# Kernel tuning notes

Hardware: AMD Instinct MI355X
Metric: run time of the kernel (lower is better)

## Reference

```python
import jax, jax.numpy as jnp
import numpy as np

B, N, S, H, W, DG = 16, 64, 4, 32, 32, 8  # batch, base width, scales, spatial, deform groups (=num_cls)
K = 9  # 3x3 kernel
EPS = 1e-5


def conv2d(x, w, b):
    # x: (B,Cin,H,W), w: (Cout,Cin,3,3), stride 1, pad 1
    y = jax.lax.conv_general_dilated(x, w, (1, 1), ((1, 1), (1, 1)),
                                     dimension_numbers=('NCHW', 'OIHW', 'NCHW'))
    return y + b[None, :, None, None]


def bn(x, g, be):
    # BatchNorm2d in training mode: batch stats over (N,H,W) per channel
    m = x.mean(axis=(0, 2, 3), keepdims=True)
    v = x.var(axis=(0, 2, 3), keepdims=True)
    return g[None, :, None, None] * (x - m) / jnp.sqrt(v + EPS) + be[None, :, None, None]


def maxpool(x):
    b, c, h, w = x.shape
    return x.reshape(b, c, h // 2, 2, w // 2, 2).max(axis=(3, 5))


def deform_conv(x, offset, w, b, dg):
    # DCNv1: x (B,Cin,H,W), offset (B,2*K*dg,H,W) laid out as [dg,k,(y,x)], w (Cout,Cin,3,3)
    Bn, Cin, Hh, Ww = x.shape
    Cp = Cin // dg
    off = offset.reshape(Bn, dg, K, 2, Hh, Ww)
    ky = (jnp.arange(K) // 3 - 1).astype(x.dtype)
    kx = (jnp.arange(K) % 3 - 1).astype(x.dtype)
    py = jnp.arange(Hh, dtype=x.dtype)[None, None, None, :, None] + ky[None, None, :, None, None] + off[:, :, :, 0]
    px = jnp.arange(Ww, dtype=x.dtype)[None, None, None, None, :] + kx[None, None, :, None, None] + off[:, :, :, 1]
    y0 = jnp.floor(py)
    x0 = jnp.floor(px)
    ly = py - y0  # (B,dg,K,H,W)
    lx = px - x0
    y0i = y0.astype(jnp.int32)
    x0i = x0.astype(jnp.int32)
    xg = x.reshape(Bn, dg, Cp, Hh * Ww)
    gather = jax.vmap(jax.vmap(lambda f, i: f[:, i]))  # f (Cp,HW), i (K,H,W) -> (Cp,K,H,W)

    def sample(yi, xi):
        valid = (yi >= 0) & (yi < Hh) & (xi >= 0) & (xi < Ww)
        idx = jnp.clip(yi, 0, Hh - 1) * Ww + jnp.clip(xi, 0, Ww - 1)
        vals = gather(xg, idx)  # (B,dg,Cp,K,H,W)
        return vals * valid[:, :, None].astype(x.dtype)

    v00 = sample(y0i, x0i)
    v01 = sample(y0i, x0i + 1)
    v10 = sample(y0i + 1, x0i)
    v11 = sample(y0i + 1, x0i + 1)
    wy = ly[:, :, None]
    wx = lx[:, :, None]
    patches = (v00 * (1 - wy) * (1 - wx) + v01 * (1 - wy) * wx
               + v10 * wy * (1 - wx) + v11 * wy * wx)
    patches = patches.reshape(Bn, Cin, K, Hh, Ww)
    out = jnp.einsum('bckhw,ock->bohw', patches, w.reshape(w.shape[0], Cin, K))
    return out + b[None, :, None, None]


def setup_inputs() -> dict:
    key = jax.random.key(0)
    ks = jax.random.split(key, 24)
    rn = lambda k, shp, s: jax.random.normal(k, shp, dtype=jnp.float32) * s
    inp = {
        'x': rn(ks[0], (B, 3, S, H, W), 1.0),
        'w1': rn(ks[1], (N, 3, 3, 3), float(np.sqrt(2.0 / (9 * 3)))),
        'b1': rn(ks[2], (N,), 0.01),
        'g1': jnp.ones((N,), jnp.float32),
        'be1': jnp.zeros((N,), jnp.float32),
        'w2': rn(ks[3], (2 * N, N, 3, 3), float(np.sqrt(2.0 / (9 * N)))),
        'b2': rn(ks[4], (2 * N,), 0.01),
        'wo1': rn(ks[5], (18 * DG, 2 * N, 3, 3), 0.01),
        'bo1': rn(ks[6], (18 * DG,), 0.01),
        'wd1': rn(ks[7], (2 * N, 2 * N, 3, 3), float(np.sqrt(2.0 / (9 * 2 * N)))),
        'bd1': jnp.ones((2 * N,), jnp.float32),
        'g2': jnp.ones((S,), jnp.float32),
        'be2': jnp.zeros((S,), jnp.float32),
        'wo2': rn(ks[8], (18 * DG, 2 * N, 3, 3), 0.01),
        'bo2': rn(ks[9], (18 * DG,), 0.01),
        'wd2': rn(ks[10], (4 * N, 2 * N, 3, 3), float(np.sqrt(2.0 / (9 * 2 * N)))),
        'bd2': jnp.ones((4 * N,), jnp.float32),
        'g3': jnp.ones((S,), jnp.float32),
        'be3': jnp.zeros((S,), jnp.float32),
        'wfc': rn(ks[11], (10, 4 * N * 64), 0.02),
        'bfc': jnp.zeros((10,), jnp.float32),
    }
    return inp


def reference(x, w1, b1, g1, be1, w2, b2, wo1, bo1, wd1, bd1, g2, be2,
              wo2, bo2, wd2, bd2, g3, be3, wfc, bfc):
    vms = lambda f: jax.vmap(f, in_axes=2, out_axes=2)  # map over scale axis
    h = vms(lambda xi: bn(jax.nn.relu(conv2d(xi, w1, b1)), g1, be1))(x)   # (B,N,S,32,32)
    h = vms(lambda xi: conv2d(xi, w2, b2))(h)                              # (B,2N,S,32,32)
    off1 = vms(lambda xi: conv2d(xi, wo1, bo1))(h)
    h = jnp.stack([deform_conv(h[:, :, i], off1[:, :, i], wd1, bd1, DG)
                   for i in range(S)], axis=2)                             # (B,2N,S,32,32)
    # per-channel BN over scale axis (BatchNorm2d(io_scales)), relu then pool
    h = jax.vmap(lambda xc: maxpool(bn(jax.nn.relu(xc), g2, be2)),
                 in_axes=1, out_axes=1)(h)                                 # (B,2N,S,16,16)
    off2 = vms(lambda xi: conv2d(xi, wo2, bo2))(h)
    h = jnp.stack([deform_conv(h[:, :, i], off2[:, :, i], wd2, bd2, DG)
                   for i in range(S)], axis=2)                             # (B,4N,S,16,16)
    h = jax.vmap(lambda xc: maxpool(bn(xc, g3, be3)),
                 in_axes=1, out_axes=1)(h)                                 # (B,4N,S,8,8)
    embedding = h
    strength = jax.nn.relu(h.max(axis=2))                                  # (B,4N,8,8)
    logits = strength.reshape(strength.shape[0], -1) @ wfc.T + bfc
    return logits, embedding
```

## Files before the change

kernel.cpp:

```cpp
#include <hip/hip_runtime.h>
#include <hip/hip_bf16.h>

#define NIMG 64

typedef __bf16 bf16x8 __attribute__((ext_vector_type(8)));
typedef float f32x4 __attribute__((ext_vector_type(4)));
typedef unsigned int u32x4 __attribute__((ext_vector_type(4)));

__device__ __forceinline__ float bfu2f(ushort u) {
    unsigned v = ((unsigned)u) << 16; float f; __builtin_memcpy(&f, &v, 4); return f;
}
__device__ __forceinline__ ushort f2bfu(float f) {
    __hip_bfloat16 h = __float2bfloat16(f); ushort u; __builtin_memcpy(&u, &h, 2); return u;
}
__device__ __forceinline__ f32x4 mfma16(bf16x8 a, bf16x8 b, f32x4 c) {
    return __builtin_amdgcn_mfma_f32_16x16x32_bf16(a, b, c, 0, 0, 0);
}

__global__ void detect_flag_kernel(const void* __restrict__ g1, int* __restrict__ flag) {
    if (threadIdx.x == 0 && blockIdx.x == 0) {
        unsigned u = *(const unsigned*)g1;
        *flag = (u == 0x3F803F80u) ? 1 : 0;
    }
}

#define NCVT 16
struct CvtDescs { const void* src[NCVT]; float* dst[NCVT]; int n[NCVT]; };
__global__ __launch_bounds__(256) void cvt_batch_kernel(CvtDescs d, const int* __restrict__ flag) {
    const int t = blockIdx.y;
    const int i = blockIdx.x * 256 + threadIdx.x;
    if (i >= d.n[t]) return;
    float v;
    if (*flag) v = bfu2f(((const ushort*)d.src[t])[i]);
    else       v = ((const float*)d.src[t])[i];
    d.dst[t][i] = v;
}

__global__ __launch_bounds__(256) void conv_wt_prep_kernel(const void* __restrict__ src,
                                                           const int* __restrict__ flag,
                                                           ushort* __restrict__ dst, int O, int C) {
    const int i = blockIdx.x * 256 + threadIdx.x;
    if (i >= O * C * 9) return;
    const int kk = i / (O * C);
    const int rem = i - kk * O * C;
    const int o = rem / C, c = rem - o * C;
    const int si = (o * C + c) * 9 + kk;
    dst[i] = (*flag) ? ((const ushort*)src)[si] : f2bfu(((const float*)src)[si]);
}

__global__ __launch_bounds__(256) void deform_wt_frag_kernel(const void* __restrict__ src,
                                                             const int* __restrict__ flag,
                                                             ushort* __restrict__ dst, int O) {
    const int i = blockIdx.x * 256 + threadIdx.x;
    if (i >= O * 1152) return;
    const int j = i & 7;
    const int lane = (i >> 3) & 63;
    const int rem = i >> 9;
    const int chunk = rem % 36;
    const int tile = rem / 36;
    const int n = lane & 15, quad = lane >> 4;
    const int oc = tile * 16 + n;
    const int k = chunk * 32 + quad * 8 + j;
    const int kk = k >> 7, c = k & 127;
    const int si = oc * 1152 + c * 9 + kk;
    dst[i] = (*flag) ? ((const ushort*)src)[si] : f2bfu(((const float*)src)[si]);
}

__global__ __launch_bounds__(256) void conv1_kernel(const float* __restrict__ xf,
                                                    const float* __restrict__ w1,
                                                    const float* __restrict__ b1,
                                                    ushort* __restrict__ h1) {
    __shared__ float wl[1728];
    const int img = blockIdx.x, b = img >> 2, s = img & 3;
    for (int i = threadIdx.x; i < 1728; i += 256) wl[i] = w1[i];
    __syncthreads();
    const int p = blockIdx.y * 256 + threadIdx.x;
    const int y = p >> 5, x = p & 31;
    float v[3][9];
#pragma unroll
    for (int c = 0; c < 3; c++)
#pragma unroll
        for (int dy = 0; dy < 3; dy++)
#pragma unroll
            for (int dx = 0; dx < 3; dx++) {
                const int gy = y + dy - 1, gx = x + dx - 1;
                v[c][dy * 3 + dx] = (gy >= 0 && gy < 32 && gx >= 0 && gx < 32)
                    ? xf[(size_t)(b * 12 + c * 4 + s) * 1024 + gy * 32 + gx] : 0.f;
            }
    ushort* op = h1 + ((size_t)img * 1024 + p) * 64;
#pragma unroll
    for (int og = 0; og < 8; og++) {
        union { u32x4 q; ushort h[8]; } U;
#pragma unroll
        for (int j = 0; j < 8; j++) {
            const int oc = og * 8 + j;
            float acc = b1[oc];
#pragma unroll
            for (int c = 0; c < 3; c++)
#pragma unroll
                for (int k = 0; k < 9; k++) acc = fmaf(v[c][k], wl[(oc * 3 + c) * 9 + k], acc);
            U.h[j] = f2bfu(fmaxf(acc, 0.f));
        }
        *(u32x4*)(op + og * 8) = U.q;
    }
}

__global__ __launch_bounds__(256) void bn1_partial_kernel(const ushort* __restrict__ h1,
                                                          float* __restrict__ pA,
                                                          float* __restrict__ pB) {
    const int bx = blockIdx.x, s = bx & 3, b = bx >> 2;
    const int img = b * 4 + s;
    const int wv = threadIdx.x >> 6, c = threadIdx.x & 63;
    float sum = 0.f, sq = 0.f;
    for (int p = wv * 256; p < wv * 256 + 256; p++) {
        const float v = bfu2f(h1[((size_t)img * 1024 + p) * 64 + c]);
        sum += v; sq = fmaf(v, v, sq);
    }
    const int o = ((s * 16 + b) * 4 + wv) * 64 + c;
    pA[o] = sum; pB[o] = sq;
}
__global__ void bn1_finish_kernel(const float* __restrict__ pA, const float* __restrict__ pB,
                                  const float* __restrict__ g, const float* __restrict__ be,
                                  float* __restrict__ scale, float* __restrict__ shift) {
    const int t = threadIdx.x;
    const int s = t >> 6, c = t & 63;
    float S = 0.f, Q = 0.f;
    for (int bw = 0; bw < 64; bw++) {
        const int o = ((s * 16 + (bw >> 2)) * 4 + (bw & 3)) * 64 + c;
        S += pA[o]; Q += pB[o];
    }
    const float n = 16.f * 1024.f;
    const float mean = S / n;
    const float var = fmaxf(Q / n - mean * mean, 0.f);
    const float inv = rsqrtf(var + 1e-5f);
    const float scv = g[c] * inv;
    scale[t] = scv;
    shift[t] = be[c] - mean * scv;
}

template <int WW, int CIN, int COUT, int OCB, bool AFFINE, bool OUT_NHWC>
__global__ __launch_bounds__(256, 2) void conv_mfma_kernel(
    const ushort* __restrict__ in, const ushort* __restrict__ wt,
    const float* __restrict__ bias, const float* __restrict__ scale,
    const float* __restrict__ shift, ushort* __restrict__ out) {
    constexpr int HW = WW * WW;
    constexpr int TROWS = (WW == 32) ? 8 : 16;
    constexpr int TW = WW + 2;
    constexpr int MT = OCB / 16;
    __shared__ __align__(16) ushort tile[(TROWS + 2) * TW * 32];
    __shared__ __align__(16) ushort wl[9 * OCB * 32];
    const int img = blockIdx.x, s = img & 3;
    const int y0 = blockIdx.y * TROWS;
    const int oc0 = blockIdx.z * OCB;
    const int tid = threadIdx.x;
    const int wv = tid >> 6, lane = tid & 63;
    const int n = lane & 15, quad = lane >> 4;
    f32x4 acc[4][MT];
#pragma unroll
    for (int t = 0; t < 4; t++)
#pragma unroll
        for (int o = 0; o < MT; o++) acc[t][o] = (f32x4){0.f, 0.f, 0.f, 0.f};

    for (int c0 = 0; c0 < CIN; c0 += 32) {
        __syncthreads();
        for (int i = tid; i < (TROWS + 2) * TW * 4; i += 256) {
            const int cg = i & 3, xy = i >> 2;
            const int x = xy % TW, y = xy / TW;
            const int gy = y0 + y - 1, gx = x - 1;
            u32x4 v = {0u, 0u, 0u, 0u};
            if (gy >= 0 && gy < WW && gx >= 0 && gx < WW) {
                v = *(const u32x4*)(in + (size_t)(img * HW + gy * WW + gx) * CIN + c0 + cg * 8);
                if (AFFINE) {
                    union { u32x4 q; ushort h[8]; } U; U.q = v;
#pragma unroll
                    for (int j = 0; j < 8; j++) {
                        const int c = c0 + cg * 8 + j;
                        U.h[j] = f2bfu(fmaf(bfu2f(U.h[j]), scale[s * CIN + c], shift[s * CIN + c]));
                    }
                    v = U.q;
                }
            }
            *(u32x4*)(tile + (y * TW + x) * 32 + cg * 8) = v;
        }
        for (int i = tid; i < 9 * OCB * 4; i += 256) {
            const int cg = i & 3, ko = i >> 2;
            const int oc = ko % OCB, kk = ko / OCB;
            u32x4 v = *(const u32x4*)(wt + (size_t)(kk * COUT + oc0 + oc) * CIN + c0 + cg * 8);
            *(u32x4*)(wl + (kk * OCB + oc) * 32 + cg * 8) = v;
        }
        __syncthreads();
#pragma unroll
        for (int kk = 0; kk < 9; kk++) {
            const int ky = kk / 3, kx = kk % 3;
            bf16x8 bfrag[4];
#pragma unroll
            for (int t = 0; t < 4; t++) {
                const int rt = (WW == 32) ? (2 * wv + (t >> 1)) : (4 * wv + t);
                const int x0 = (WW == 32) ? ((t & 1) * 16) : 0;
                bfrag[t] = *(const bf16x8*)(tile + ((rt + ky) * TW + x0 + n + kx) * 32 + quad * 8);
            }
#pragma unroll
            for (int o = 0; o < MT; o++) {
                const bf16x8 afrag = *(const bf16x8*)(wl + (kk * OCB + o * 16 + n) * 32 + quad * 8);
#pragma unroll
                for (int t = 0; t < 4; t++) acc[t][o] = mfma16(afrag, bfrag[t], acc[t][o]);
            }
        }
    }
#pragma unroll
    for (int t = 0; t < 4; t++) {
        const int rt = (WW == 32) ? (2 * wv + (t >> 1)) : (4 * wv + t);
        const int x0 = (WW == 32) ? ((t & 1) * 16) : 0;
        const int py = y0 + rt, px = x0 + n;
#pragma unroll
        for (int o = 0; o < MT; o++)
#pragma unroll
            for (int r = 0; r < 4; r++) {
                const int oc = oc0 + o * 16 + quad * 4 + r;
                const float v = acc[t][o][r] + bias[oc];
                if (OUT_NHWC) out[(size_t)(img * HW + py * WW + px) * COUT + oc] = f2bfu(v);
                else          out[((size_t)img * COUT + oc) * HW + py * WW + px] = f2bfu(v);
            }
    }
}

template <int COUT, int OCB, int HH, int WW>
__global__ __launch_bounds__(256, 4) void deform_direct_kernel(
    const ushort* __restrict__ in, const ushort* __restrict__ off,
    const ushort* __restrict__ wpf, const float* __restrict__ bias,
    ushort* __restrict__ out) {
    constexpr int HW = HH * WW;
    constexpr int QT = OCB / 16;
    const int img = blockIdx.x;
    const int p0 = blockIdx.y * 64;
    const int tile0 = blockIdx.z * QT;
    const int tid = threadIdx.x;
    const int wv = tid >> 6, lane = tid & 63;
    const int n = lane & 15, quad = lane >> 4;
    const int p = p0 + wv * 16 + n;
    const int yy = p / WW, xx = p % WW;

    f32x4 acc[QT];
#pragma unroll
    for (int t = 0; t < QT; t++) acc[t] = (f32x4){0.f, 0.f, 0.f, 0.f};
    const ushort* wbase = wpf + ((size_t)tile0 * 36) * 512 + lane * 8;
    const ushort* ibase = in + (size_t)img * HW * 128;
    const ushort* obase = off + (size_t)img * 144 * HW + p;

#pragma unroll 2
    for (int chunk = 0; chunk < 36; chunk++) {
        const int gk = chunk * 32 + quad * 8;
        const int kk = gk >> 7;
        const int dg = (gk & 127) >> 4;
        const int cp0 = gk & 15;
        const int ch = dg * 9 + kk;
        const float offy = bfu2f(obase[(ch * 2 + 0) * HW]);
        const float offx = bfu2f(obase[(ch * 2 + 1) * HW]);
        const float py = (float)(yy + kk / 3 - 1) + offy;
        const float pxf = (float)(xx + kk % 3 - 1) + offx;
        const float y0f = floorf(py), x0f = floorf(pxf);
        const float ly = py - y0f, lx = pxf - x0f;
        const int iy0 = (int)y0f, ix0 = (int)x0f;
        const int iy1 = iy0 + 1, ix1 = ix0 + 1;
        const bool vy0 = iy0 >= 0 && iy0 < HH, vy1 = iy1 >= 0 && iy1 < HH;
        const bool vx0 = ix0 >= 0 && ix0 < WW, vx1 = ix1 >= 0 && ix1 < WW;
        const int cy0 = min(max(iy0, 0), HH - 1), cy1 = min(max(iy1, 0), HH - 1);
        const int cx0 = min(max(ix0, 0), WW - 1), cx1 = min(max(ix1, 0), WW - 1);
        const float w00 = (1.f - ly) * (1.f - lx) * ((vy0 && vx0) ? 1.f : 0.f);
        const float w01 = (1.f - ly) * lx * ((vy0 && vx1) ? 1.f : 0.f);
        const float w10 = ly * (1.f - lx) * ((vy1 && vx0) ? 1.f : 0.f);
        const float w11 = ly * lx * ((vy1 && vx1) ? 1.f : 0.f);
        const ushort* cbase = ibase + dg * 16 + cp0;
        union { u32x4 q; ushort h[8]; } A0, A1, A2, A3, R;
        A0.q = *(const u32x4*)(cbase + (size_t)(cy0 * WW + cx0) * 128);
        A1.q = *(const u32x4*)(cbase + (size_t)(cy0 * WW + cx1) * 128);
        A2.q = *(const u32x4*)(cbase + (size_t)(cy1 * WW + cx0) * 128);
        A3.q = *(const u32x4*)(cbase + (size_t)(cy1 * WW + cx1) * 128);
#pragma unroll
        for (int j = 0; j < 8; j++) {
            float v = w00 * bfu2f(A0.h[j]);
            v = fmaf(w01, bfu2f(A1.h[j]), v);
            v = fmaf(w10, bfu2f(A2.h[j]), v);
            v = fmaf(w11, bfu2f(A3.h[j]), v);
            R.h[j] = f2bfu(v);
        }
        const bf16x8 afrag = *(const bf16x8*)&R;
#pragma unroll
        for (int t = 0; t < QT; t++) {
            const bf16x8 bfrag = *(const bf16x8*)(wbase + ((size_t)(t * 36 + chunk)) * 512);
            acc[t] = mfma16(afrag, bfrag, acc[t]);
        }
    }
#pragma unroll
    for (int t = 0; t < QT; t++) {
        const int oc = (tile0 + t) * 16 + n;
        const float bv = bias[oc];
        union { uint2 q; ushort h4[4]; } U;
#pragma unroll
        for (int r = 0; r < 4; r++) U.h4[r] = f2bfu(acc[t][r] + bv);
        *(uint2*)(out + ((size_t)img * COUT + oc) * HW + p0 + wv * 16 + quad * 4) = U.q;
    }
}

__global__ __launch_bounds__(256) void bn_stats_plane_kernel(
    const ushort* __restrict__ in, int C, int HW, int relu_in,
    const float* __restrict__ gamma, const float* __restrict__ beta,
    float* __restrict__ scale, float* __restrict__ shift) {
    const int g = blockIdx.x;
    const int s = g / C, c = g % C;
    float sum = 0.f, sq = 0.f;
    for (int b = 0; b < 16; b++) {
        const ushort* p = in + ((size_t)(b * 4 + s) * C + c) * HW;
        for (int i = threadIdx.x; i < HW; i += 256) {
            float v = bfu2f(p[i]);
            if (relu_in) v = fmaxf(v, 0.f);
            sum += v; sq = fmaf(v, v, sq);
        }
    }
    for (int o = 32; o > 0; o >>= 1) {
        sum += __shfl_down(sum, o, 64);
        sq += __shfl_down(sq, o, 64);
    }
    __shared__ float as_[4], aq_[4];
    const int wave = threadIdx.x >> 6, lane = threadIdx.x & 63;
    if (lane == 0) { as_[wave] = sum; aq_[wave] = sq; }
    __syncthreads();
    if (threadIdx.x == 0) {
        const float nn = 16.f * (float)HW;
        const float S_ = as_[0] + as_[1] + as_[2] + as_[3];
        const float Q_ = aq_[0] + aq_[1] + aq_[2] + aq_[3];
        const float mean = S_ / nn;
        const float var = fmaxf(Q_ / nn - mean * mean, 0.f);
        const float inv = rsqrtf(var + 1e-5f);
        const float scv = gamma[s] * inv;
        scale[g] = scv;
        shift[g] = beta[s] - mean * scv;
    }
}

__global__ __launch_bounds__(256) void bn_pool_nhwc_kernel(
    const ushort* __restrict__ in, ushort* __restrict__ out,
    const float* __restrict__ scale, const float* __restrict__ shift) {
    const int idx = blockIdx.x * 256 + threadIdx.x;
    const int c = idx & 127;
    const int p = (idx >> 7) & 255;
    const int img = idx >> 15;
    const int s = img & 3;
    const int oy = p >> 4, ox = p & 15;
    const float sc = scale[s * 128 + c], sh = shift[s * 128 + c];
    const ushort* ip = in + ((size_t)img * 128 + c) * 1024 + (2 * oy) * 32 + 2 * ox;
    float m = -3.4e38f;
#pragma unroll
    for (int dy = 0; dy < 2; dy++)
#pragma unroll
        for (int dx = 0; dx < 2; dx++) {
            float v = fmaxf(bfu2f(ip[dy * 32 + dx]), 0.f);
            m = fmaxf(m, fmaf(v, sc, sh));
        }
    out[((size_t)img * 256 + p) * 128 + c] = f2bfu(m);
}

__global__ __launch_bounds__(256) void bn_pool_embed_kernel(
    const ushort* __restrict__ in, void* __restrict__ out, const int* __restrict__ flag,
    float* __restrict__ p2, const float* __restrict__ scale, const float* __restrict__ shift) {
    const int idx = blockIdx.x * 256 + threadIdx.x;
    const int p = idx & 63;
    const int c = (idx >> 6) & 255;
    const int img = idx >> 14;
    const int b = img >> 2, s = img & 3;
    const int oy = p >> 3, ox = p & 7;
    const float sc = scale[s * 256 + c], sh = shift[s * 256 + c];
    const ushort* ip = in + ((size_t)img * 256 + c) * 256 + (2 * oy) * 16 + 2 * ox;
    float m = fmaxf(fmaf(bfu2f(ip[0]), sc, sh), fmaf(bfu2f(ip[1]), sc, sh));
    m = fmaxf(m, fmaf(bfu2f(ip[16]), sc, sh));
    m = fmaxf(m, fmaf(bfu2f(ip[17]), sc, sh));
    p2[idx] = m;
    const size_t eidx = 160 + (((size_t)(b * 256 + c) * 4 + s) * 64) + p;
    if (*flag) ((ushort*)out)[eidx] = f2bfu(m);
    else       ((float*)out)[eidx] = m;
}

__global__ __launch_bounds__(256) void strength_kernel(const float* __restrict__ p2,
                                                       float* __restrict__ st) {
    const int idx = blockIdx.x * 256 + threadIdx.x;
    const int p = idx & 63;
    const int c = (idx >> 6) & 255;
    const int b = idx >> 14;
    const float* e = p2 + ((size_t)(b * 4) * 256 + c) * 64 + p;
    float m = fmaxf(fmaxf(e[0], e[16384]), fmaxf(e[2 * 16384], e[3 * 16384]));
    st[idx] = fmaxf(m, 0.f);
}

__global__ __launch_bounds__(256) void fc_kernel(const float* __restrict__ st,
                                                 const float* __restrict__ wfc,
                                                 const float* __restrict__ bfc,
                                                 void* __restrict__ out,
                                                 const int* __restrict__ flag) {
    const int b = blockIdx.x / 10, o = blockIdx.x % 10;
    const float* sp = st + (size_t)b * 16384;
    const float* wpp = wfc + (size_t)o * 16384;
    float sum = 0.f;
    for (int i = threadIdx.x; i < 16384; i += 256) sum = fmaf(sp[i], wpp[i], sum);
    for (int off = 32; off > 0; off >>= 1) sum += __shfl_down(sum, off, 64);
    __shared__ float ws4[4];
    const int wave = threadIdx.x >> 6, lane = threadIdx.x & 63;
    if (lane == 0) ws4[wave] = sum;
    __syncthreads();
    if (threadIdx.x == 0) {
        const float r = ws4[0] + ws4[1] + ws4[2] + ws4[3] + bfc[o];
        if (*flag) ((ushort*)out)[b * 10 + o] = f2bfu(r);
        else       ((float*)out)[b * 10 + o] = r;
    }
}

extern "C" void kernel_launch(void* const* d_in, const int* in_sizes, int n_in,
                              void* d_out, int out_size, void* d_ws, size_t ws_size,
                              hipStream_t stream) {
    (void)in_sizes; (void)n_in; (void)out_size; (void)ws_size;
    float* ws = (float*)d_ws;
    ushort* wsh = (ushort*)d_ws;
    int* flagp = (int*)d_ws;

    float* xf   = ws + 16;
    float* w1f  = ws + 196624;
    float* b1f  = ws + 198352;
    float* g1f  = ws + 198416;
    float* be1f = ws + 198480;
    float* b2f  = ws + 198544;
    float* bo1f = ws + 198672;
    float* bd1f = ws + 198816;
    float* bo2f = ws + 198944;
    float* bd2f = ws + 199088;
    float* g2f  = ws + 199344; float* be2f = ws + 199348;
    float* g3f  = ws + 199352; float* be3f = ws + 199356;
    float* wfcf = ws + 199360;
    float* bfcf = ws + 363200;
    float* sc1  = ws + 363216; float* sh1 = ws + 363472;
    float* sc2  = ws + 363728; float* sh2 = ws + 364240;
    float* sc3  = ws + 364752; float* sh3 = ws + 365776;
    float* pA   = ws + 366800;
    float* pB   = ws + 383184;
    ushort* w2t  = wsh + 799136;
    ushort* wo1t = wsh + 872864;
    ushort* wo2t = wsh + 1038752;
    ushort* wd1p = wsh + 1204640;
    ushort* wd2p = wsh + 1352096;
    ushort* h1   = wsh + 1647008;
    ushort* h2   = wsh + 5841312;
    ushort* off1 = wsh + 14229920;
    ushort* d1   = wsh + 23667104;
    ushort* p1   = wsh + 1647008;
    ushort* off2 = wsh + 5841312;
    ushort* d2   = wsh + 14229920;
    float* p2    = ws + 11833552;
    float* strg  = ws + 12882128;

    detect_flag_kernel<<<1, 64, 0, stream>>>(d_in[3], flagp);
    CvtDescs cd;
    const int srcIdx[NCVT] = {0, 1, 2, 3, 4, 6, 8, 10, 11, 12, 14, 16, 17, 18, 19, 20};
    float* dsts[NCVT] = {xf, w1f, b1f, g1f, be1f, b2f, bo1f, bd1f, g2f, be2f,
                         bo2f, bd2f, g3f, be3f, wfcf, bfcf};
    const int ns[NCVT] = {196608, 1728, 64, 64, 64, 128, 144, 128, 4, 4,
                          144, 256, 4, 4, 163840, 10};
    for (int i = 0; i < NCVT; i++) { cd.src[i] = d_in[srcIdx[i]]; cd.dst[i] = dsts[i]; cd.n[i] = ns[i]; }
    cvt_batch_kernel<<<dim3(768, NCVT), 256, 0, stream>>>(cd, flagp);
    conv_wt_prep_kernel<<<288, 256, 0, stream>>>(d_in[5], flagp, w2t, 128, 64);
    conv_wt_prep_kernel<<<648, 256, 0, stream>>>(d_in[7], flagp, wo1t, 144, 128);
    conv_wt_prep_kernel<<<648, 256, 0, stream>>>(d_in[13], flagp, wo2t, 144, 128);
    deform_wt_frag_kernel<<<576, 256, 0, stream>>>(d_in[9], flagp, wd1p, 128);
    deform_wt_frag_kernel<<<1152, 256, 0, stream>>>(d_in[15], flagp, wd2p, 256);

    conv1_kernel<<<dim3(NIMG, 4), 256, 0, stream>>>(xf, w1f, b1f, h1);
    bn1_partial_kernel<<<64, 256, 0, stream>>>(h1, pA, pB);
    bn1_finish_kernel<<<1, 256, 0, stream>>>(pA, pB, g1f, be1f, sc1, sh1);
    conv_mfma_kernel<32, 64, 128, 64, true, true>
        <<<dim3(NIMG, 4, 2), 256, 0, stream>>>(h1, w2t, b2f, sc1, sh1, h2);
    conv_mfma_kernel<32, 128, 144, 48, false, false>
        <<<dim3(NIMG, 4, 3), 256, 0, stream>>>(h2, wo1t, bo1f, nullptr, nullptr, off1);
    deform_direct_kernel<128, 128, 32, 32>
        <<<dim3(NIMG, 16, 1), 256, 0, stream>>>(h2, off1, wd1p, bd1f, d1);
    bn_stats_plane_kernel<<<512, 256, 0, stream>>>(d1, 128, 1024, 1, g2f, be2f, sc2, sh2);
    bn_pool_nhwc_kernel<<<8192, 256, 0, stream>>>(d1, p1, sc2, sh2);

    conv_mfma_kernel<16, 128, 144, 48, false, false>
        <<<dim3(NIMG, 1, 3), 256, 0, stream>>>(p1, wo2t, bo2f, nullptr, nullptr, off2);
    deform_direct_kernel<256, 128, 16, 16>
        <<<dim3(NIMG, 4, 2), 256, 0, stream>>>(p1, off2, wd2p, bd2f, d2);
    bn_stats_plane_kernel<<<1024, 256, 0, stream>>>(d2, 256, 256, 0, g3f, be3f, sc3, sh3);
    bn_pool_embed_kernel<<<4096, 256, 0, stream>>>(d2, d_out, flagp, p2, sc3, sh3);

    strength_kernel<<<1024, 256, 0, stream>>>(p2, strg);
    fc_kernel<<<160, 256, 0, stream>>>(strg, wfcf, bfcf, d_out, flagp);
}
```

Baseline: 436.0 us.

## Store deform inputs in deform-group-planar layout for gather locality

Measured after the change: 392.4 us, median of 2. 1.11x faster.

```diff
diff --git a/kernel.cpp b/kernel.cpp
--- a/kernel.cpp
+++ b/kernel.cpp
@@ -138,7 +138,7 @@
     shift[t] = be[c] - mean * scv;
 }
 
-template <int WW, int CIN, int COUT, int OCB, bool AFFINE, bool OUT_NHWC>
+template <int WW, int CIN, int COUT, int OCB, bool AFFINE, bool IN_DGP, bool OUT_DGP>
 __global__ __launch_bounds__(256, 2) void conv_mfma_kernel(
     const ushort* __restrict__ in, const ushort* __restrict__ wt,
     const float* __restrict__ bias, const float* __restrict__ scale,
@@ -169,13 +169,16 @@
             const int gy = y0 + y - 1, gx = x - 1;
             u32x4 v = {0u, 0u, 0u, 0u};
             if (gy >= 0 && gy < WW && gx >= 0 && gx < WW) {
-                v = *(const u32x4*)(in + (size_t)(img * HW + gy * WW + gx) * CIN + c0 + cg * 8);
+                const int c = c0 + cg * 8;
+                size_t addr;
+                if (IN_DGP) addr = ((size_t)(img * 8 + (c >> 4)) * HW + gy * WW + gx) * 16 + (c & 15);
+                else        addr = (size_t)(img * HW + gy * WW + gx) * CIN + c;
+                v = *(const u32x4*)(in + addr);
                 if (AFFINE) {
                     union { u32x4 q; ushort h[8]; } U; U.q = v;
 #pragma unroll
                     for (int j = 0; j < 8; j++) {
-                        const int c = c0 + cg * 8 + j;
-                        U.h[j] = f2bfu(fmaf(bfu2f(U.h[j]), scale[s * CIN + c], shift[s * CIN + c]));
+                        U.h[j] = f2bfu(fmaf(bfu2f(U.h[j]), scale[s * CIN + c + j], shift[s * CIN + c + j]));
                     }
                     v = U.q;
                 }
@@ -218,8 +221,10 @@
             for (int r = 0; r < 4; r++) {
                 const int oc = oc0 + o * 16 + quad * 4 + r;
                 const float v = acc[t][o][r] + bias[oc];
-                if (OUT_NHWC) out[(size_t)(img * HW + py * WW + px) * COUT + oc] = f2bfu(v);
-                else          out[((size_t)img * COUT + oc) * HW + py * WW + px] = f2bfu(v);
+                if (OUT_DGP)
+                    out[((size_t)(img * 8 + (oc >> 4)) * HW + py * WW + px) * 16 + (oc & 15)] = f2bfu(v);
+                else
+                    out[((size_t)img * COUT + oc) * HW + py * WW + px] = f2bfu(v);
             }
     }
 }
@@ -244,7 +249,6 @@
 #pragma unroll
     for (int t = 0; t < QT; t++) acc[t] = (f32x4){0.f, 0.f, 0.f, 0.f};
     const ushort* wbase = wpf + ((size_t)tile0 * 36) * 512 + lane * 8;
-    const ushort* ibase = in + (size_t)img * HW * 128;
     const ushort* obase = off + (size_t)img * 144 * HW + p;
 
 #pragma unroll 2
@@ -270,12 +274,12 @@
         const float w01 = (1.f - ly) * lx * ((vy0 && vx1) ? 1.f : 0.f);
         const float w10 = ly * (1.f - lx) * ((vy1 && vx0) ? 1.f : 0.f);
         const float w11 = ly * lx * ((vy1 && vx1) ? 1.f : 0.f);
-        const ushort* cbase = ibase + dg * 16 + cp0;
+        const ushort* cbase = in + ((size_t)(img * 8 + dg) * HW) * 16 + cp0;
         union { u32x4 q; ushort h[8]; } A0, A1, A2, A3, R;
-        A0.q = *(const u32x4*)(cbase + (size_t)(cy0 * WW + cx0) * 128);
-        A1.q = *(const u32x4*)(cbase + (size_t)(cy0 * WW + cx1) * 128);
-        A2.q = *(const u32x4*)(cbase + (size_t)(cy1 * WW + cx0) * 128);
-        A3.q = *(const u32x4*)(cbase + (size_t)(cy1 * WW + cx1) * 128);
+        A0.q = *(const u32x4*)(cbase + (size_t)(cy0 * WW + cx0) * 16);
+        A1.q = *(const u32x4*)(cbase + (size_t)(cy0 * WW + cx1) * 16);
+        A2.q = *(const u32x4*)(cbase + (size_t)(cy1 * WW + cx0) * 16);
+        A3.q = *(const u32x4*)(cbase + (size_t)(cy1 * WW + cx1) * 16);
 #pragma unroll
         for (int j = 0; j < 8; j++) {
             float v = w00 * bfu2f(A0.h[j]);
@@ -338,7 +342,7 @@
     }
 }
 
-__global__ __launch_bounds__(256) void bn_pool_nhwc_kernel(
+__global__ __launch_bounds__(256) void bn_pool_dgp_kernel(
     const ushort* __restrict__ in, ushort* __restrict__ out,
     const float* __restrict__ scale, const float* __restrict__ shift) {
     const int idx = blockIdx.x * 256 + threadIdx.x;
@@ -357,7 +361,7 @@
             float v = fmaxf(bfu2f(ip[dy * 32 + dx]), 0.f);
             m = fmaxf(m, fmaf(v, sc, sh));
         }
-    out[((size_t)img * 256 + p) * 128 + c] = f2bfu(m);
+    out[((size_t)(img * 8 + (c >> 4)) * 256 + p) * 16 + (c & 15)] = f2bfu(m);
 }
 
 __global__ __launch_bounds__(256) void bn_pool_embed_kernel(
@@ -473,16 +477,16 @@
     conv1_kernel<<<dim3(NIMG, 4), 256, 0, stream>>>(xf, w1f, b1f, h1);
     bn1_partial_kernel<<<64, 256, 0, stream>>>(h1, pA, pB);
     bn1_finish_kernel<<<1, 256, 0, stream>>>(pA, pB, g1f, be1f, sc1, sh1);
-    conv_mfma_kernel<32, 64, 128, 64, true, true>
+    conv_mfma_kernel<32, 64, 128, 64, true, false, true>
         <<<dim3(NIMG, 4, 2), 256, 0, stream>>>(h1, w2t, b2f, sc1, sh1, h2);
-    conv_mfma_kernel<32, 128, 144, 48, false, false>
+    conv_mfma_kernel<32, 128, 144, 48, false, true, false>
         <<<dim3(NIMG, 4, 3), 256, 0, stream>>>(h2, wo1t, bo1f, nullptr, nullptr, off1);
     deform_direct_kernel<128, 128, 32, 32>
         <<<dim3(NIMG, 16, 1), 256, 0, stream>>>(h2, off1, wd1p, bd1f, d1);
     bn_stats_plane_kernel<<<512, 256, 0, stream>>>(d1, 128, 1024, 1, g2f, be2f, sc2, sh2);
-    bn_pool_nhwc_kernel<<<8192, 256, 0, stream>>>(d1, p1, sc2, sh2);
-
-    conv_mfma_kernel<16, 128, 144, 48, false, false>
+    bn_pool_dgp_kernel<<<8192, 256, 0, stream>>>(d1, p1, sc2, sh2);
+
+    conv_mfma_kernel<16, 128, 144, 48, false, true, false>
         <<<dim3(NIMG, 1, 3), 256, 0, stream>>>(p1, wo2t, bo2f, nullptr, nullptr, off2);
     deform_direct_kernel<256, 128, 16, 16>
         <<<dim3(NIMG, 4, 2), 256, 0, stream>>>(p1, off2, wd2p, bd2f, d2);
```
